# Kernel optimization log

Hardware: AMD Instinct MI355X
Metric: run time of the kernel (lower is better)

Reference implementation:

```python
import jax, jax.numpy as jnp
import numpy as np
from math import comb

N, D, ORDER, P = 32768, 8, 19, 20
O = ORDER + 1


def bernstein(X, order):
    # X: [N, D] in [0,1] -> Bernstein basis [N, D, order+1]
    o = order + 1
    r = jnp.arange(o, dtype=X.dtype)
    binom = jnp.asarray([comb(order, k) for k in range(o)], dtype=X.dtype)
    Xe = X[..., None]
    return (Xe ** r) * ((1.0 - Xe) ** (order - r)) * binom


def setup_inputs() -> dict:
    key = jax.random.key(0)
    k0, k1, k2, k3, k4, k5 = jax.random.split(key, 6)
    X = jax.random.uniform(k0, (N, D), dtype=jnp.float32)
    # perm: each row is a permutation of range(D) (as in the module default)
    perm = jax.vmap(lambda k: jax.random.permutation(k, D))(jax.random.split(k1, P)).astype(jnp.int32)
    meanw0 = -0.2 + 0.1 * jax.random.normal(k2, (P, 1, O), dtype=jnp.float32)
    meanw = -0.2 + 0.1 * jax.random.normal(k3, (D - 1, P, O, O), dtype=jnp.float32)
    varw0 = 0.05 * jax.random.normal(k4, (P, 1, O), dtype=jnp.float32)
    varw = 0.05 * jax.random.normal(k5, (D - 1, P, O, O), dtype=jnp.float32)
    return {"X": X, "perm": perm, "meanw0": meanw0, "meanw": meanw,
            "varw0": varw0, "varw": varw}


def reference(X, perm, meanw0, meanw, varw0, varw):
    outB = bernstein(X, ORDER)                       # [N, D, O]
    outBp = jnp.transpose(outB[:, perm], (1, 0, 2, 3))  # gather axis=1 -> [P, N, D, O]

    # ---- f_mean: chain of small matmuls with exp(meanw_i), gated by basis ----
    f = jnp.exp(meanw0) * outBp[:, :, 0, :]          # [P,1,O]*[P,N,O] -> [P,N,O]
    for i in range(1, D):
        f = jnp.einsum('pno,poq->pnq', f, jnp.exp(meanw[i - 1])) * outBp[:, :, i, :]
    mean = jnp.sum(jnp.sum(f, axis=-1), axis=0)[:, None]   # [N,1]

    # ---- f_var: six moment chains one..six, exp(meanw)^2 * exp(varw)^k ----
    kk = jnp.arange(1, 7, dtype=X.dtype).reshape(6, 1, 1, 1)
    B2_0 = outBp[:, :, 0, :] ** 2                    # [P,N,O]
    acc = jnp.exp(2.0 * meanw0 + kk * varw0) * B2_0[None]  # [6,P,N,O]
    for i in range(1, D):
        Wi = jnp.exp(2.0 * meanw[i - 1] + kk * varw[i - 1])  # [6,P,O,O]
        acc = jnp.einsum('kpno,kpoq->kpnq', acc, Wi) * (outBp[:, :, i, :] ** 2)[None]
    mom = jnp.sum(acc, axis=-1)                      # [6,P,N]
    c = jnp.asarray([1.0, 1 / 2, 1 / 6, 1 / 24, 1 / 120, 1 / 720], dtype=X.dtype)
    var = jnp.einsum('k,kpn->n', c, mom)[:, None]    # [N,1]

    return jnp.concatenate([mean, var], axis=-1)     # [N,2]
```

## Files before the change

### kernel.cpp

```cpp
#include <hip/hip_runtime.h>
#include <math.h>

#define NPTS 32768
#define DD 8
#define OO 20
#define PP 20
#define NCHAIN 7
#define NT 2

typedef _Float16 half8 __attribute__((ext_vector_type(8)));
typedef __fp16 fp16x2 __attribute__((ext_vector_type(2)));
typedef float floatx16 __attribute__((ext_vector_type(16)));

__device__ __forceinline__ int sigma_row(int m) {
    return (m >= 4 && m < 12) ? (m ^ 12) : m;
}

__device__ __forceinline__ void basis20(float tv, float* g) {
    constexpr float binom[OO] = {
        1.f, 19.f, 171.f, 969.f, 3876.f, 11628.f, 27132.f, 50388.f, 75582.f,
        92378.f, 92378.f, 75582.f, 50388.f, 27132.f, 11628.f, 3876.f, 969.f,
        171.f, 19.f, 1.f};
    float a = tv, b = 1.f - tv, v = 1.f;
#pragma unroll
    for (int q = 0; q < OO; ++q) { g[q] = v; v *= a; }
    v = 1.f;
#pragma unroll
    for (int q = OO - 1; q >= 0; --q) { g[q] = g[q] * v * binom[q]; v *= b; }
}

__device__ __forceinline__ unsigned pk2rtn(float a, float b) {
    union { _Float16 h[2]; unsigned u; } cv;
    cv.h[0] = (_Float16)a; cv.h[1] = (_Float16)b;
    return cv.u;
}

__device__ __forceinline__ unsigned pack_pk(float x, float y) {
    union { fp16x2 h; unsigned u; } cv;
    cv.h = __builtin_amdgcn_cvt_pkrtz(x, y);
    return cv.u;
}

__device__ __forceinline__ fp16x2 u2h(unsigned u) {
    union { unsigned u; fp16x2 h; } c; c.u = u; return c.h;
}
__device__ __forceinline__ unsigned h2u(fp16x2 h) {
    union { unsigned u; fp16x2 h; } c; c.h = h; return c.u;
}

__global__ void prep_kernel(const float* __restrict__ X,
                            const float* __restrict__ meanw0,
                            const float* __restrict__ meanw,
                            const float* __restrict__ varw0,
                            const float* __restrict__ varw,
                            float* __restrict__ W0,
                            _Float16* __restrict__ WA,
                            unsigned* __restrict__ G) {
    int e = blockIdx.x * 256 + threadIdx.x;
    const int n0 = NCHAIN * PP * OO;
    const int nW = NCHAIN * (DD - 1) * PP * 32 * 32;
    const int nG = NPTS * DD;
    if (e < n0) {
        int q = e % OO;
        int rem = e / OO;
        int p = rem % PP;
        int c = rem / PP;
        float m = meanw0[p * OO + q];
        W0[e] = (c == 0) ? __expf(m) : __expf(2.f * m + (float)c * varw0[p * OO + q]);
    } else if (e < n0 + nW) {
        int idx = e - n0;
        int k = idx & 31; idx >>= 5;
        int m = idx & 31; idx >>= 5;
        int p = idx % PP; idx /= PP;
        int i = idx % (DD - 1);
        int c = idx / (DD - 1);
        int q = sigma_row(m);
        float v = 0.f;
        if (q < OO && k < OO) {
            int mi = ((i * PP + p) * OO + k) * OO + q;
            float mm = meanw[mi];
            v = (c == 0) ? __expf(mm) : __expf(2.f * mm + (float)c * varw[mi]);
        }
        WA[e - n0] = (_Float16)v;
    } else if (e < n0 + nW + nG) {
        int idx = e - n0 - nW;
        int n = idx & (NPTS - 1);
        int d = idx >> 15;
        float g[OO];
        basis20(X[(size_t)n * DD + d], g);
        float lo[12], hi12[12];
#pragma unroll
        for (int r = 0; r < 8; ++r) lo[r] = g[r];
#pragma unroll
        for (int r = 0; r < 4; ++r) lo[8 + r] = g[16 + r];
#pragma unroll
        for (int r = 0; r < 8; ++r) hi12[r] = g[8 + r];
#pragma unroll
        for (int r = 0; r < 4; ++r) hi12[8 + r] = 0.f;
        unsigned rec[24];
#pragma unroll
        for (int q = 0; q < 6; ++q) {
            rec[q]      = pk2rtn(lo[2 * q], lo[2 * q + 1]);
            rec[6 + q]  = pk2rtn(lo[2 * q] * lo[2 * q], lo[2 * q + 1] * lo[2 * q + 1]);
            rec[12 + q] = pk2rtn(hi12[2 * q], hi12[2 * q + 1]);
            rec[18 + q] = pk2rtn(hi12[2 * q] * hi12[2 * q], hi12[2 * q + 1] * hi12[2 * q + 1]);
        }
        uint4* out = (uint4*)(G + (size_t)(d * NPTS + n) * 24);
#pragma unroll
        for (int q = 0; q < 6; ++q) out[q] = ((const uint4*)rec)[q];
    }
}

__global__ __launch_bounds__(256, 2) void chain_kernel(
    const int* __restrict__ perm,
    const float* __restrict__ W0, const _Float16* __restrict__ WA,
    const unsigned* __restrict__ G, float* __restrict__ partial) {
    const int lane = threadIdx.x & 63;
    const int wv = threadIdx.x >> 6;
    const int nl = lane & 31;
    const bool hi = (lane >> 5) != 0;
    const int n0 = (blockIdx.x * 4 + wv) * (32 * NT);
    const int p = blockIdx.y;
    const int goff = hi ? 12 : 0;

    int dp[DD];
#pragma unroll
    for (int i = 0; i < DD; ++i) dp[i] = perm[p * DD + i];

    const unsigned uz = ((unsigned)dp[0]) >> 20;
    const float fz = __uint_as_float(uz);
    floatx16 kZero;
#pragma unroll
    for (int r = 0; r < 16; ++r) kZero[r] = fz;

    unsigned st[NT][NCHAIN][6];

#pragma unroll
    for (int tile = 0; tile < NT; ++tile) {
        const uint4* rp = (const uint4*)(
            G + ((size_t)dp[0] * NPTS + (n0 + tile * 32 + nl)) * 24 + goff);
        uint4 r0 = rp[0], r1 = rp[1], r2 = rp[2];
        unsigned gw[6] = {r0.x, r0.y, r0.z, r0.w, r1.x, r1.y};
        unsigned sw[6] = {r1.z, r1.w, r2.x, r2.y, r2.z, r2.w};
        float gcf[12], scf[12];
#pragma unroll
        for (int q = 0; q < 6; ++q) {
            fp16x2 gh = u2h(gw[q]), sh = u2h(sw[q]);
            gcf[2 * q] = (float)gh.x; gcf[2 * q + 1] = (float)gh.y;
            scf[2 * q] = (float)sh.x; scf[2 * q + 1] = (float)sh.y;
        }
#pragma unroll
        for (int c = 0; c < NCHAIN; ++c) {
            const float* w0r = W0 + (c * PP + p) * OO;
            float val[12];
#pragma unroll
            for (int r = 0; r < 8; ++r) {
                float ws = hi ? w0r[r + 8] : w0r[r];
                val[r] = ws * (c == 0 ? gcf[r] : scf[r]);
            }
#pragma unroll
            for (int r = 8; r < 12; ++r) {
                float ws = hi ? 0.f : w0r[r + 8];
                val[r] = ws * (c == 0 ? gcf[r] : scf[r]);
            }
#pragma unroll
            for (int e = 0; e < 6; ++e)
                st[tile][c][e] = pack_pk(val[2 * e], val[2 * e + 1]);
        }
    }

    const int aoff = nl * 32 + (hi ? 8 : 0);
    const float coef[NCHAIN] = {0.f, 1.f, 0.5f, 1.f / 6.f, 1.f / 24.f,
                                1.f / 120.f, 1.f / 720.f};
    float sm[NT], sv[NT];
#pragma unroll
    for (int tile = 0; tile < NT; ++tile) { sm[tile] = 0.f; sv[tile] = 0.f; }

#pragma unroll
    for (int i = 1; i < DD; ++i) {
        unsigned gw[NT][6], sw[NT][6];
#pragma unroll
        for (int tile = 0; tile < NT; ++tile) {
            const uint4* rp = (const uint4*)(
                G + ((size_t)dp[i] * NPTS + (n0 + tile * 32 + nl)) * 24 + goff);
            uint4 r0 = rp[0], r1 = rp[1], r2 = rp[2];
            gw[tile][0] = r0.x; gw[tile][1] = r0.y; gw[tile][2] = r0.z;
            gw[tile][3] = r0.w; gw[tile][4] = r1.x; gw[tile][5] = r1.y;
            sw[tile][0] = r1.z; sw[tile][1] = r1.w; sw[tile][2] = r2.x;
            sw[tile][3] = r2.y; sw[tile][4] = r2.z; sw[tile][5] = r2.w;
        }

        float gcf[NT][12], scf[NT][12];
        if (i == DD - 1) {
#pragma unroll
            for (int tile = 0; tile < NT; ++tile)
#pragma unroll
                for (int q = 0; q < 6; ++q) {
                    fp16x2 gh = u2h(gw[tile][q]), sh = u2h(sw[tile][q]);
                    gcf[tile][2 * q] = (float)gh.x; gcf[tile][2 * q + 1] = (float)gh.y;
                    scf[tile][2 * q] = (float)sh.x; scf[tile][2 * q + 1] = (float)sh.y;
                }
        }

#pragma unroll
        for (int c = 0; c < NCHAIN; ++c) {
            const _Float16* wa =
                WA + (size_t)(((c * (DD - 1)) + (i - 1)) * PP + p) * 1024 + aoff;
            half8 A0 = *(const half8*)(wa);
            half8 A1 = *(const half8*)(wa + 16);

#pragma unroll
            for (int tile = 0; tile < NT; ++tile) {
                union { unsigned u[4]; half8 h; } B0, B1;
                B0.u[0] = st[tile][c][0]; B0.u[1] = st[tile][c][1];
                B0.u[2] = st[tile][c][2]; B0.u[3] = st[tile][c][3];
                B1.u[0] = st[tile][c][4]; B1.u[1] = st[tile][c][5];
                B1.u[2] = uz;             B1.u[3] = uz;

                floatx16 acc;
                acc = __builtin_amdgcn_mfma_f32_32x32x16_f16(A0, B0.h, kZero, 0, 0, 0);
                acc = __builtin_amdgcn_mfma_f32_32x32x16_f16(A1, B1.h, acc, 0, 0, 0);

                if (i < DD - 1) {
#pragma unroll
                    for (int e = 0; e < 6; ++e) {
                        fp16x2 pr = __builtin_amdgcn_cvt_pkrtz(acc[2 * e], acc[2 * e + 1]);
                        fp16x2 gv = u2h(c == 0 ? gw[tile][e] : sw[tile][e]);
                        st[tile][c][e] = h2u(pr * gv);
                    }
                } else {
                    float s = 0.f;
#pragma unroll
                    for (int r = 0; r < 12; ++r)
                        s += acc[r] * (c == 0 ? gcf[tile][r] : scf[tile][r]);
                    if (c == 0) sm[tile] = s;
                    else        sv[tile] += coef[c] * s;
                }
            }
        }
    }

#pragma unroll
    for (int tile = 0; tile < NT; ++tile) {
        float m = sm[tile] + __shfl_xor(sm[tile], 32, 64);
        float v = sv[tile] + __shfl_xor(sv[tile], 32, 64);
        if (lane < 32) {
            partial[(size_t)p * NPTS + n0 + tile * 32 + nl] = m;
            partial[(size_t)(PP + p) * NPTS + n0 + tile * 32 + nl] = v;
        }
    }
}

__global__ void reduce_kernel(const float* __restrict__ partial,
                              float* __restrict__ out) {
    int n = blockIdx.x * 256 + threadIdx.x;
    float m = 0.f, v = 0.f;
#pragma unroll
    for (int p = 0; p < PP; ++p) {
        m += partial[(size_t)p * NPTS + n];
        v += partial[(size_t)(PP + p) * NPTS + n];
    }
    out[2 * n] = m;
    out[2 * n + 1] = v;
}

extern "C" void kernel_launch(void* const* d_in, const int* in_sizes, int n_in,
                              void* d_out, int out_size, void* d_ws, size_t ws_size,
                              hipStream_t stream) {
    const float* X      = (const float*)d_in[0];
    const int*   perm   = (const int*)d_in[1];
    const float* meanw0 = (const float*)d_in[2];
    const float* meanw  = (const float*)d_in[3];
    const float* varw0  = (const float*)d_in[4];
    const float* varw   = (const float*)d_in[5];
    float* out = (float*)d_out;

    float*     W0      = (float*)d_ws;
    _Float16*  WA      = (_Float16*)((char*)d_ws + 11200);
    float*     partial = (float*)((char*)d_ws + 11200 + 2007040);
    unsigned*  G       = (unsigned*)((char*)d_ws + 11200 + 2007040 + 5242880);

    int prep_n = NCHAIN * PP * OO + NCHAIN * (DD - 1) * PP * 32 * 32 + NPTS * DD;
    hipLaunchKernelGGL(prep_kernel, dim3((prep_n + 255) / 256), dim3(256), 0,
                       stream, X, meanw0, meanw, varw0, varw, W0, WA, G);

    dim3 grid(NPTS / (128 * NT), PP);
    hipLaunchKernelGGL(chain_kernel, grid, dim3(256), 0, stream,
                       perm, W0, WA, G, partial);

    hipLaunchKernelGGL(reduce_kernel, dim3(NPTS / 256), dim3(256), 0, stream,
                       partial, out);
}
```

Measured before the change: 174.1 us.

## Stage MFMA weight fragments in double-buffered LDS via async global_load_lds

Changes the precomputed fp16 weight layout so that each 16-byte lane fragment sits contiguously in fragment order. The chain kernel then streams each layer's seven chain weight matrices into a double-buffered shared-memory region with global_load_lds, prefetching layer i+1 while computing layer i. The goal is to replace per-wave redundant global reads of weights with one block-wide async copy, overlapped with compute. In exchange it adds LDS usage (about 28 KB per block) and block barriers each layer, which may reduce occupancy.

```diff
diff --git a/kernel.cpp b/kernel.cpp
--- a/kernel.cpp
+++ b/kernel.cpp
@@ -11,6 +11,10 @@
 typedef _Float16 half8 __attribute__((ext_vector_type(8)));
 typedef __fp16 fp16x2 __attribute__((ext_vector_type(2)));
 typedef float floatx16 __attribute__((ext_vector_type(16)));
+typedef unsigned int u32;
+
+#define AS1 __attribute__((address_space(1)))
+#define AS3 __attribute__((address_space(3)))
 
 __device__ __forceinline__ int sigma_row(int m) {
     return (m >= 4 && m < 12) ? (m ^ 12) : m;
@@ -69,11 +73,14 @@
         W0[e] = (c == 0) ? __expf(m) : __expf(2.f * m + (float)c * varw0[p * OO + q]);
     } else if (e < n0 + nW) {
         int idx = e - n0;
-        int k = idx & 31; idx >>= 5;
-        int m = idx & 31; idx >>= 5;
+        int j = idx & 7; idx >>= 3;
+        int l = idx & 63; idx >>= 6;
+        int f = idx & 1; idx >>= 1;
         int p = idx % PP; idx /= PP;
         int i = idx % (DD - 1);
         int c = idx / (DD - 1);
+        int m = l & 31;
+        int k = (l >> 5) * 8 + f * 16 + j;
         int q = sigma_row(m);
         float v = 0.f;
         if (q < OO && k < OO) {
@@ -123,6 +130,8 @@
     const int p = blockIdx.y;
     const int goff = hi ? 12 : 0;
 
+    __shared__ __align__(16) _Float16 Alds[2][NCHAIN * 1024];
+
     int dp[DD];
 #pragma unroll
     for (int i = 0; i < DD; ++i) dp[i] = perm[p * DD + i];
@@ -132,6 +141,18 @@
     floatx16 kZero;
 #pragma unroll
     for (int r = 0; r < 16; ++r) kZero[r] = fz;
+
+    {
+        const _Float16* wbase = WA + (size_t)p * 1024;
+#pragma unroll
+        for (int u = wv; u < 2 * NCHAIN; u += 4) {
+            int c = u >> 1, h = u & 1;
+            const _Float16* src =
+                wbase + (size_t)c * (DD - 1) * PP * 1024 + h * 512 + lane * 8;
+            __builtin_amdgcn_global_load_lds(
+                (const AS1 u32*)src, (AS3 u32*)&Alds[0][u * 512], 16, 0, 0);
+        }
+    }
 
     unsigned st[NT][NCHAIN][6];
 
@@ -169,15 +190,30 @@
         }
     }
 
-    const int aoff = nl * 32 + (hi ? 8 : 0);
     const float coef[NCHAIN] = {0.f, 1.f, 0.5f, 1.f / 6.f, 1.f / 24.f,
                                 1.f / 120.f, 1.f / 720.f};
     float sm[NT], sv[NT];
 #pragma unroll
     for (int tile = 0; tile < NT; ++tile) { sm[tile] = 0.f; sv[tile] = 0.f; }
 
+    __syncthreads();
+
 #pragma unroll
     for (int i = 1; i < DD; ++i) {
+        const int cur = (i - 1) & 1;
+
+        if (i < DD - 1) {
+            const _Float16* wbase = WA + (size_t)(i * PP + p) * 1024;
+#pragma unroll
+            for (int u = wv; u < 2 * NCHAIN; u += 4) {
+                int c = u >> 1, h = u & 1;
+                const _Float16* src =
+                    wbase + (size_t)c * (DD - 1) * PP * 1024 + h * 512 + lane * 8;
+                __builtin_amdgcn_global_load_lds(
+                    (const AS1 u32*)src, (AS3 u32*)&Alds[cur ^ 1][u * 512], 16, 0, 0);
+            }
+        }
+
         unsigned gw[NT][6], sw[NT][6];
 #pragma unroll
         for (int tile = 0; tile < NT; ++tile) {
@@ -204,10 +240,9 @@
 
 #pragma unroll
         for (int c = 0; c < NCHAIN; ++c) {
-            const _Float16* wa =
-                WA + (size_t)(((c * (DD - 1)) + (i - 1)) * PP + p) * 1024 + aoff;
-            half8 A0 = *(const half8*)(wa);
-            half8 A1 = *(const half8*)(wa + 16);
+            const _Float16* ab = &Alds[cur][c * 1024 + lane * 8];
+            half8 A0 = *(const half8*)(ab);
+            half8 A1 = *(const half8*)(ab + 512);
 
 #pragma unroll
             for (int tile = 0; tile < NT; ++tile) {
@@ -238,6 +273,8 @@
                 }
             }
         }
+
+        if (i < DD - 1) __syncthreads();
     }
 
 #pragma unroll
```

Result: faster. 158.4 us (-9.0%).
